# Kernel optimization log

Hardware: AMD Instinct MI355X
Metric: run time of the kernel (lower is better)

The kernel has to match this reference:

```python
import jax, jax.numpy as jnp
import numpy as np

B, T_V, T_A = 128, 64, 128
E_V, E_A = 1024, 512
H, EMB, C = 1024, 512, 512  # C = input_size - embedding_size
IN = EMB + C               # RNN input size = 1024
VOCAB = 20000


def setup_inputs() -> dict:
    key = jax.random.key(0)
    ks = jax.random.split(key, 26)
    s = 0.02
    inp = {
        "input": jax.random.normal(ks[0], (B, 1, EMB), jnp.float32),
        "enc_visual": jax.random.normal(ks[1], (B, T_V, E_V), jnp.float32),
        "enc_audio": jax.random.normal(ks[2], (B, T_A, E_A), jnp.float32),
        "hidden_state": jax.random.normal(ks[3], (1, B, H), jnp.float32),
        "cell_state": jax.random.normal(ks[4], (1, B, H), jnp.float32),
        # visual attention (Bahdanau): W1:[C,H], W2:[C,E_V], W3:[1,C]
        "W_va1": s * jax.random.normal(ks[5], (C, H), jnp.float32),
        "W_va2": s * jax.random.normal(ks[6], (C, E_V), jnp.float32),
        "W_va3": s * jax.random.normal(ks[7], (1, C), jnp.float32),
        "W_venc": s * jax.random.normal(ks[8], (C, E_V), jnp.float32),
        # audio attention
        "W_aa1": s * jax.random.normal(ks[9], (C, H), jnp.float32),
        "W_aa2": s * jax.random.normal(ks[10], (C, E_A), jnp.float32),
        "W_aa3": s * jax.random.normal(ks[11], (1, C), jnp.float32),
        "W_aenc": s * jax.random.normal(ks[12], (C, E_A), jnp.float32),
        # cross-modal context attention (over 2 context vectors)
        "W_ca1": s * jax.random.normal(ks[13], (C, H), jnp.float32),
        "W_ca2": s * jax.random.normal(ks[14], (C, C), jnp.float32),
        "W_ca3": s * jax.random.normal(ks[15], (1, C), jnp.float32),
        # LSTM-style custom RNN cell params
        "W_ih": s * jax.random.normal(ks[16], (4 * H, IN), jnp.float32),
        "W_hh": s * jax.random.normal(ks[17], (4 * H, H), jnp.float32),
        "b_ih": jnp.zeros((4 * H,), jnp.float32),
        "b_hh": jnp.zeros((4 * H,), jnp.float32),
        # output projection
        "W_out": s * jax.random.normal(ks[18], (VOCAB, H), jnp.float32),
        "b_out": jnp.zeros((VOCAB,), jnp.float32),
    }
    return inp


def _attend(h, enc, W1, W2, W3):
    # h: [B,H]; enc: [B,T,E]. Vectorized Bahdanau attention (original loops over T).
    v1 = h @ W1.T                               # [B,C]
    v2 = jnp.einsum('bte,ce->btc', enc, W2)     # [B,T,C]
    scores = jnp.tanh(v1[:, None, :] + v2) @ W3.T  # [B,T,1]
    attn = jax.nn.softmax(scores[..., 0], axis=1)  # [B,T]
    return jnp.einsum('bt,bte->be', attn, enc)     # [B,E]


def reference(input, enc_visual, enc_audio, hidden_state, cell_state,
              W_va1, W_va2, W_va3, W_venc,
              W_aa1, W_aa2, W_aa3, W_aenc,
              W_ca1, W_ca2, W_ca3,
              W_ih, W_hh, b_ih, b_hh, W_out, b_out):
    h0 = hidden_state[0]   # [B,H]
    c0 = cell_state[0]     # [B,H]

    vc = _attend(h0, enc_visual, W_va1, W_va2, W_va3) @ W_venc.T  # [B,C]
    ac = _attend(h0, enc_audio, W_aa1, W_aa2, W_aa3) @ W_aenc.T   # [B,C]
    all_ctx = jnp.stack([vc, ac], axis=1)                         # [B,2,C]
    final_ctx = _attend(h0, all_ctx, W_ca1, W_ca2, W_ca3)         # [B,C]

    x = jnp.concatenate([input[:, 0, :], jnp.tanh(final_ctx)], axis=-1)  # [B,IN]
    gates = x @ W_ih.T + b_ih + h0 @ W_hh.T + b_hh                 # [B,4H]
    i, f, g, o = jnp.split(gates, 4, axis=-1)
    c_new = jax.nn.sigmoid(f) * c0 + jax.nn.sigmoid(i) * jnp.tanh(g)
    h_new = jax.nn.sigmoid(o) * jnp.tanh(c_new)

    logits = h_new @ W_out.T + b_out                               # [B,V]
    return (logits[:, None, :], h_new[None], c_new[None])
```

## Files before the change

kernel.cpp:

```cpp
#include <hip/hip_runtime.h>
#include <hip/hip_bf16.h>
#include <cstddef>

typedef __attribute__((ext_vector_type(8))) short short8;
typedef __attribute__((ext_vector_type(4))) float f32x4;

#define LSTR 40

static __device__ __forceinline__ short8 pack8(float4 f0, float4 f1) {
    union { __hip_bfloat162 h[4]; short8 s; } u;
    u.h[0] = __float22bfloat162_rn(make_float2(f0.x, f0.y));
    u.h[1] = __float22bfloat162_rn(make_float2(f0.z, f0.w));
    u.h[2] = __float22bfloat162_rn(make_float2(f1.x, f1.y));
    u.h[3] = __float22bfloat162_rn(make_float2(f1.z, f1.w));
    return u.s;
}

static __device__ __forceinline__ void sk_body(
    const float* __restrict__ A, int lda,
    const float* __restrict__ W,
    const float* __restrict__ bias, int addbias,
    float* __restrict__ C, int ldc, int N,
    int kbeg, int kend, int n0, int m0)
{
    __shared__ short As[128 * LSTR];
    __shared__ short Ws[64 * LSTR];
    const int tid  = threadIdx.x;
    const int lane = tid & 63;
    const int wave = tid >> 6;
    const int wm = wave * 32;

    f32x4 acc[2][4];
    #pragma unroll
    for (int i = 0; i < 2; ++i)
        #pragma unroll
        for (int j = 0; j < 4; ++j)
            acc[i][j] = (f32x4){0.f, 0.f, 0.f, 0.f};

    const int srow  = tid >> 2;
    const int skoff = (tid & 3) * 8;
    const int frow  = lane & 15;
    const int fkoff = (lane >> 4) * 8;

    for (int k0 = kbeg; k0 < kend; k0 += 32) {
        #pragma unroll
        for (int p = 0; p < 2; ++p) {
            int row = srow + p * 64;
            const float* sa = A + (size_t)(m0 + row) * lda + k0 + skoff;
            *(short8*)(As + row * LSTR + skoff) =
                pack8(*(const float4*)sa, *(const float4*)(sa + 4));
        }
        {
            int n = n0 + srow;
            short8 v = (short8){0,0,0,0,0,0,0,0};
            if (n < N) {
                const float* sw = W + (size_t)n * lda + k0 + skoff;
                v = pack8(*(const float4*)sw, *(const float4*)(sw + 4));
            }
            *(short8*)(Ws + srow * LSTR + skoff) = v;
        }
        __syncthreads();

        short8 af[2], bf[4];
        #pragma unroll
        for (int i = 0; i < 2; ++i)
            af[i] = *(const short8*)(As + (wm + i * 16 + frow) * LSTR + fkoff);
        #pragma unroll
        for (int j = 0; j < 4; ++j)
            bf[j] = *(const short8*)(Ws + (j * 16 + frow) * LSTR + fkoff);
        #pragma unroll
        for (int i = 0; i < 2; ++i)
            #pragma unroll
            for (int j = 0; j < 4; ++j)
                acc[i][j] = __builtin_amdgcn_mfma_f32_16x16x32_bf16(af[i], bf[j], acc[i][j], 0, 0, 0);
        __syncthreads();
    }

    const int cl = lane & 15;
    const int rq = (lane >> 4) * 4;
    #pragma unroll
    for (int j = 0; j < 4; ++j) {
        int gc = n0 + j * 16 + cl;
        if (gc >= N) continue;
        float b = addbias ? bias[gc] : 0.f;
        #pragma unroll
        for (int i = 0; i < 2; ++i) {
            int gr = m0 + wm + i * 16 + rq;
            #pragma unroll
            for (int r = 0; r < 4; ++r)
                atomicAdd(C + (size_t)(gr + r) * ldc + gc, acc[i][j][r] + b);
        }
    }
}

__global__ __launch_bounds__(256) void gemm_sk(
    const float* __restrict__ A, const float* __restrict__ W,
    const float* __restrict__ bias, float* __restrict__ C,
    int N, int K, int kchunk, int ldc)
{
    int kbeg = blockIdx.y * kchunk;
    sk_body(A, K, W, bias, bias != nullptr && blockIdx.y == 0,
            C, ldc, N, kbeg, kbeg + kchunk, blockIdx.x * 64, blockIdx.z * 128);
}

__global__ __launch_bounds__(256) void hproj3_mfma(
    const float* __restrict__ h0,
    const float* __restrict__ Wa, const float* __restrict__ Wb, const float* __restrict__ Wc,
    float* __restrict__ hbase)
{
    int n0g = blockIdx.x * 64;
    int wsel = n0g >> 9;
    const float* W = (wsel == 0) ? Wa : (wsel == 1) ? Wb : Wc;
    float* C = hbase + (size_t)wsel * 128 * 512;
    int kbeg = blockIdx.y * 256;
    sk_body(h0, 1024, W, nullptr, 0, C, 512, 512, kbeg, kbeg + 256, n0g & 511, 0);
}

__global__ __launch_bounds__(256) void ctxproj_mfma(
    const float* __restrict__ attv, const float* __restrict__ Wv,
    const float* __restrict__ atta, const float* __restrict__ Wa,
    float* __restrict__ ctx)
{
    const float* A; const float* W; float* C; int lda, kb, ke;
    if (blockIdx.z == 0) { A = attv; W = Wv; C = ctx;       lda = 1024; kb = blockIdx.y * 256; ke = kb + 256; }
    else                 { A = atta; W = Wa; C = ctx + 512; lda = 512;  kb = blockIdx.y * 128; ke = kb + 128; }
    sk_body(A, lda, W, nullptr, 0, C, 1024, 512, kb, ke, blockIdx.x * 64, 0);
}

__global__ __launch_bounds__(256) void gates_mfma(
    const float* __restrict__ xb, const float* __restrict__ W_ih,
    const float* __restrict__ h0, const float* __restrict__ W_hh,
    float* __restrict__ gates)
{
    int pair = blockIdx.y >> 1;
    const float* A = pair ? h0 : xb;
    const float* W = pair ? W_hh : W_ih;
    int kb = (blockIdx.y & 1) * 512;
    sk_body(A, 1024, W, nullptr, 0, gates, 4096, 4096, kb, kb + 512, blockIdx.x * 64, 0);
}

__global__ __launch_bounds__(256) void gemm_scores(
    const float* __restrict__ A, const float* __restrict__ W,
    const float* __restrict__ v1, const float* __restrict__ W3,
    float* __restrict__ sc, int N, int K, int tshift)
{
    __shared__ short As[128 * LSTR];
    __shared__ short Ws[128 * LSTR];
    const int tid  = threadIdx.x;
    const int lane = tid & 63;
    const int wave = tid >> 6;
    const int m0 = blockIdx.y * 128;
    const int n0 = blockIdx.x * 128;
    const int wm = (wave >> 1) * 64;
    const int wn = (wave & 1) * 64;

    f32x4 acc[4][4];
    #pragma unroll
    for (int i = 0; i < 4; ++i)
        #pragma unroll
        for (int j = 0; j < 4; ++j)
            acc[i][j] = (f32x4){0.f, 0.f, 0.f, 0.f};

    const int srow  = tid >> 2;
    const int skoff = (tid & 3) * 8;
    const int frow  = lane & 15;
    const int fkoff = (lane >> 4) * 8;

    for (int k0 = 0; k0 < K; k0 += 32) {
        #pragma unroll
        for (int p = 0; p < 2; ++p) {
            int row = srow + p * 64;
            const float* sa = A + (size_t)(m0 + row) * K + k0 + skoff;
            *(short8*)(As + row * LSTR + skoff) =
                pack8(*(const float4*)sa, *(const float4*)(sa + 4));
            const float* sw = W + (size_t)(n0 + row) * K + k0 + skoff;
            *(short8*)(Ws + row * LSTR + skoff) =
                pack8(*(const float4*)sw, *(const float4*)(sw + 4));
        }
        __syncthreads();

        short8 af[4], bf[4];
        #pragma unroll
        for (int i = 0; i < 4; ++i)
            af[i] = *(const short8*)(As + (wm + i * 16 + frow) * LSTR + fkoff);
        #pragma unroll
        for (int j = 0; j < 4; ++j)
            bf[j] = *(const short8*)(Ws + (wn + j * 16 + frow) * LSTR + fkoff);
        #pragma unroll
        for (int i = 0; i < 4; ++i)
            #pragma unroll
            for (int j = 0; j < 4; ++j)
                acc[i][j] = __builtin_amdgcn_mfma_f32_16x16x32_bf16(af[i], bf[j], acc[i][j], 0, 0, 0);
        __syncthreads();
    }

    const int cl = lane & 15;
    const int rq = (lane >> 4) * 4;
    #pragma unroll
    for (int i = 0; i < 4; ++i) {
        #pragma unroll
        for (int r = 0; r < 4; ++r) {
            int gr = m0 + wm + i * 16 + rq + r;
            const float* v1row = v1 + (size_t)(gr >> tshift) * 512;
            float p = 0.f;
            #pragma unroll
            for (int j = 0; j < 4; ++j) {
                int gc = n0 + wn + j * 16 + cl;
                p += tanhf(v1row[gc] + acc[i][j][r]) * W3[gc];
            }
            p += __shfl_xor(p, 1, 64);
            p += __shfl_xor(p, 2, 64);
            p += __shfl_xor(p, 4, 64);
            p += __shfl_xor(p, 8, 64);
            if (cl == 0) atomicAdd(sc + gr, p);
        }
    }
}

__global__ __launch_bounds__(256) void attend_out_kernel(
    const float* __restrict__ sc, const float* __restrict__ enc,
    float* __restrict__ out, int T, int E)
{
    __shared__ float raw[128];
    __shared__ float ew[128];
    const int b = blockIdx.x, tid = threadIdx.x;
    if (tid < T) raw[tid] = sc[(size_t)b * T + tid];
    __syncthreads();
    float m = -1e30f;
    for (int t = 0; t < T; ++t) m = fmaxf(m, raw[t]);
    if (tid < T) ew[tid] = __expf(raw[tid] - m);
    __syncthreads();
    float sum = 0.f;
    for (int t = 0; t < T; ++t) sum += ew[t];
    const float inv = 1.f / sum;

    const int e = blockIdx.y * 256 + tid;
    const float* encb = enc + (size_t)b * T * E + e;
    float acc = 0.f;
    for (int t = 0; t < T; ++t)
        acc += ew[t] * encb[(size_t)t * E];
    out[(size_t)b * E + e] = acc * inv;
}

__global__ __launch_bounds__(256) void cross_kernel(
    const float* __restrict__ hc1, const float* __restrict__ v2c,
    const float* __restrict__ W3, const float* __restrict__ ctx,
    const float* __restrict__ inp, float* __restrict__ x)
{
    const int C = 512;
    __shared__ float red[256];
    __shared__ float aw[2];
    const int b = blockIdx.x, tid = threadIdx.x;

    float p0 = 0.f, p1 = 0.f;
    for (int c = tid; c < C; c += 256) {
        float h = hc1[(size_t)b * C + c], w = W3[c];
        p0 += tanhf(h + v2c[(size_t)(b * 2 + 0) * C + c]) * w;
        p1 += tanhf(h + v2c[(size_t)(b * 2 + 1) * C + c]) * w;
    }
    red[tid] = p0; __syncthreads();
    for (int s = 128; s; s >>= 1) { if (tid < s) red[tid] += red[tid + s]; __syncthreads(); }
    float s0 = red[0];
    __syncthreads();
    red[tid] = p1; __syncthreads();
    for (int s = 128; s; s >>= 1) { if (tid < s) red[tid] += red[tid + s]; __syncthreads(); }
    if (tid == 0) {
        float s1 = red[0];
        float m = fmaxf(s0, s1);
        float e0 = __expf(s0 - m), e1 = __expf(s1 - m);
        float inv = 1.f / (e0 + e1);
        aw[0] = e0 * inv; aw[1] = e1 * inv;
    }
    __syncthreads();
    float a0 = aw[0], a1 = aw[1];
    for (int c = tid; c < C; c += 256) {
        float fc = a0 * ctx[(size_t)(b * 2 + 0) * C + c]
                 + a1 * ctx[(size_t)(b * 2 + 1) * C + c];
        x[(size_t)b * 1024 + 512 + c] = tanhf(fc);
        x[(size_t)b * 1024 + c] = inp[(size_t)b * 512 + c];
    }
}

__global__ __launch_bounds__(256) void lstm_kernel(
    const float* __restrict__ gates, const float* __restrict__ c0,
    const float* __restrict__ b_ih, const float* __restrict__ b_hh,
    float* __restrict__ hout, float* __restrict__ cout)
{
    const int idx = blockIdx.x * 256 + threadIdx.x;
    const int b = idx >> 10, h = idx & 1023;
    const float* g = gates + (size_t)b * 4096;
    float gi = g[h]        + b_ih[h]        + b_hh[h];
    float gf = g[1024 + h] + b_ih[1024 + h] + b_hh[1024 + h];
    float gg = g[2048 + h] + b_ih[2048 + h] + b_hh[2048 + h];
    float go = g[3072 + h] + b_ih[3072 + h] + b_hh[3072 + h];
    float si = 1.f / (1.f + __expf(-gi));
    float sf = 1.f / (1.f + __expf(-gf));
    float so = 1.f / (1.f + __expf(-go));
    float cn = sf * c0[idx] + si * tanhf(gg);
    float hn = so * tanhf(cn);
    cout[idx] = cn;
    hout[idx] = hn;
}

extern "C" void kernel_launch(void* const* d_in, const int* in_sizes, int n_in,
                              void* d_out, int out_size, void* d_ws, size_t ws_size,
                              hipStream_t stream)
{
    const float* inp    = (const float*)d_in[0];
    const float* encv   = (const float*)d_in[1];
    const float* enca   = (const float*)d_in[2];
    const float* h0     = (const float*)d_in[3];
    const float* c0     = (const float*)d_in[4];
    const float* W_va1  = (const float*)d_in[5];
    const float* W_va2  = (const float*)d_in[6];
    const float* W_va3  = (const float*)d_in[7];
    const float* W_venc = (const float*)d_in[8];
    const float* W_aa1  = (const float*)d_in[9];
    const float* W_aa2  = (const float*)d_in[10];
    const float* W_aa3  = (const float*)d_in[11];
    const float* W_aenc = (const float*)d_in[12];
    const float* W_ca1  = (const float*)d_in[13];
    const float* W_ca2  = (const float*)d_in[14];
    const float* W_ca3  = (const float*)d_in[15];
    const float* W_ih   = (const float*)d_in[16];
    const float* W_hh   = (const float*)d_in[17];
    const float* b_ih   = (const float*)d_in[18];
    const float* b_hh   = (const float*)d_in[19];
    const float* W_out  = (const float*)d_in[20];
    const float* b_out  = (const float*)d_in[21];
    float* out = (float*)d_out;

    float* ws = (float*)d_ws;
    float* hv1  = ws;  ws += 128 * 512;
    float* ha1  = ws;  ws += 128 * 512;
    float* hc1  = ws;  ws += 128 * 512;
    float* scv  = ws;  ws += 128 * 64;
    float* sca  = ws;  ws += 128 * 128;
    float* ctx  = ws;  ws += 128 * 2 * 512;
    float* v2c  = ws;  ws += 128 * 2 * 512;
    float* gates= ws;  ws += (size_t)128 * 4096;
    size_t zero_floats = (size_t)(ws - (float*)d_ws);
    float* xb   = ws;  ws += 128 * 1024;
    float* attv = ws;  ws += 128 * 1024;
    float* atta = ws;  ws += 128 * 512;

    dim3 blk(256);

    hipMemsetAsync(d_ws, 0, zero_floats * sizeof(float), stream);
    hipMemsetAsync(out, 0, (size_t)128 * 20000 * sizeof(float), stream);

    hproj3_mfma<<<dim3(24, 4), blk, 0, stream>>>(h0, W_va1, W_aa1, W_ca1, hv1);
    gemm_scores<<<dim3(4, 64),  blk, 0, stream>>>(encv, W_va2, hv1, W_va3, scv, 512, 1024, 6);
    gemm_scores<<<dim3(4, 128), blk, 0, stream>>>(enca, W_aa2, ha1, W_aa3, sca, 512,  512, 7);
    attend_out_kernel<<<dim3(128, 4), blk, 0, stream>>>(scv, encv, attv, 64, 1024);
    attend_out_kernel<<<dim3(128, 2), blk, 0, stream>>>(sca, enca, atta, 128, 512);
    ctxproj_mfma<<<dim3(8, 4, 2), blk, 0, stream>>>(attv, W_venc, atta, W_aenc, ctx);
    gemm_sk<<<dim3(8, 2, 2), blk, 0, stream>>>(ctx, W_ca2, nullptr, v2c, 512, 512, 256, 512);
    cross_kernel<<<128, blk, 0, stream>>>(hc1, v2c, W_ca3, ctx, inp, xb);
    gates_mfma<<<dim3(64, 4), blk, 0, stream>>>(xb, W_ih, h0, W_hh, gates);
    float* hout = out + 2560000;
    float* cout = out + 2560000 + 131072;
    lstm_kernel<<<512, blk, 0, stream>>>(gates, c0, b_ih, b_hh, hout, cout);
    gemm_sk<<<dim3(313, 2, 1), blk, 0, stream>>>(hout, W_out, b_out, out, 20000, 1024, 512, 20000);
}
```

Baseline: 457.8 us.

## Merge visual/audio score GEMMs and attend kernels, deepen split-K for small GEMMs

Fuses the two attention score GEMMs into one launch with 64-row M tiles, giving 1536 blocks instead of 768, and fuses the two softmax-weighted sum kernels into one launch. It also doubles the split-K factor for the hidden projection, the context projection, the cross-attention projection and the gates GEMM so more workgroups cover the GPU. This cuts launch count and raises occupancy on the many-CU MI355X. The cost is more atomic accumulation traffic and less reuse of the W tile per block.

```diff
diff --git a/kernel.cpp b/kernel.cpp
--- a/kernel.cpp
+++ b/kernel.cpp
@@ -112,8 +112,8 @@
     int wsel = n0g >> 9;
     const float* W = (wsel == 0) ? Wa : (wsel == 1) ? Wb : Wc;
     float* C = hbase + (size_t)wsel * 128 * 512;
-    int kbeg = blockIdx.y * 256;
-    sk_body(h0, 1024, W, nullptr, 0, C, 512, 512, kbeg, kbeg + 256, n0g & 511, 0);
+    int kbeg = blockIdx.y * 128;
+    sk_body(h0, 1024, W, nullptr, 0, C, 512, 512, kbeg, kbeg + 128, n0g & 511, 0);
 }
 
 __global__ __launch_bounds__(256) void ctxproj_mfma(
@@ -122,8 +122,8 @@
     float* __restrict__ ctx)
 {
     const float* A; const float* W; float* C; int lda, kb, ke;
-    if (blockIdx.z == 0) { A = attv; W = Wv; C = ctx;       lda = 1024; kb = blockIdx.y * 256; ke = kb + 256; }
-    else                 { A = atta; W = Wa; C = ctx + 512; lda = 512;  kb = blockIdx.y * 128; ke = kb + 128; }
+    if (blockIdx.z == 0) { A = attv; W = Wv; C = ctx;       lda = 1024; kb = blockIdx.y * 128; ke = kb + 128; }
+    else                 { A = atta; W = Wa; C = ctx + 512; lda = 512;  kb = blockIdx.y * 64;  ke = kb + 64;  }
     sk_body(A, lda, W, nullptr, 0, C, 1024, 512, kb, ke, blockIdx.x * 64, 0);
 }
 
@@ -132,31 +132,48 @@
     const float* __restrict__ h0, const float* __restrict__ W_hh,
     float* __restrict__ gates)
 {
-    int pair = blockIdx.y >> 1;
+    int pair = blockIdx.y >> 2;
     const float* A = pair ? h0 : xb;
     const float* W = pair ? W_hh : W_ih;
-    int kb = (blockIdx.y & 1) * 512;
-    sk_body(A, 1024, W, nullptr, 0, gates, 4096, 4096, kb, kb + 512, blockIdx.x * 64, 0);
-}
-
-__global__ __launch_bounds__(256) void gemm_scores(
-    const float* __restrict__ A, const float* __restrict__ W,
-    const float* __restrict__ v1, const float* __restrict__ W3,
-    float* __restrict__ sc, int N, int K, int tshift)
-{
-    __shared__ short As[128 * LSTR];
+    int kb = (blockIdx.y & 3) * 256;
+    sk_body(A, 1024, W, nullptr, 0, gates, 4096, 4096, kb, kb + 256, blockIdx.x * 64, 0);
+}
+
+__global__ __launch_bounds__(256) void scores_fused(
+    const float* __restrict__ encv, const float* __restrict__ W_va2,
+    const float* __restrict__ hv1,  const float* __restrict__ W_va3,
+    float* __restrict__ scv,
+    const float* __restrict__ enca, const float* __restrict__ W_aa2,
+    const float* __restrict__ ha1,  const float* __restrict__ W_aa3,
+    float* __restrict__ sca)
+{
+    __shared__ short As[64 * LSTR];
     __shared__ short Ws[128 * LSTR];
+
+    const float *A, *W, *v1, *W3;
+    float* sc;
+    int K, tshift, n0, m0;
+    int idx = blockIdx.x;
+    if (idx < 512) {
+        n0 = (idx >> 7) * 128;  m0 = (idx & 127) * 64;
+        A = encv; W = W_va2; v1 = hv1; W3 = W_va3; sc = scv;
+        K = 1024; tshift = 6;
+    } else {
+        idx -= 512;
+        n0 = (idx >> 8) * 128;  m0 = (idx & 255) * 64;
+        A = enca; W = W_aa2; v1 = ha1; W3 = W_aa3; sc = sca;
+        K = 512; tshift = 7;
+    }
+
     const int tid  = threadIdx.x;
     const int lane = tid & 63;
     const int wave = tid >> 6;
-    const int m0 = blockIdx.y * 128;
-    const int n0 = blockIdx.x * 128;
-    const int wm = (wave >> 1) * 64;
+    const int wm = (wave >> 1) * 32;
     const int wn = (wave & 1) * 64;
 
-    f32x4 acc[4][4];
+    f32x4 acc[2][4];
     #pragma unroll
-    for (int i = 0; i < 4; ++i)
+    for (int i = 0; i < 2; ++i)
         #pragma unroll
         for (int j = 0; j < 4; ++j)
             acc[i][j] = (f32x4){0.f, 0.f, 0.f, 0.f};
@@ -167,27 +184,29 @@
     const int fkoff = (lane >> 4) * 8;
 
     for (int k0 = 0; k0 < K; k0 += 32) {
+        {
+            const float* sa = A + (size_t)(m0 + srow) * K + k0 + skoff;
+            *(short8*)(As + srow * LSTR + skoff) =
+                pack8(*(const float4*)sa, *(const float4*)(sa + 4));
+        }
         #pragma unroll
         for (int p = 0; p < 2; ++p) {
             int row = srow + p * 64;
-            const float* sa = A + (size_t)(m0 + row) * K + k0 + skoff;
-            *(short8*)(As + row * LSTR + skoff) =
-                pack8(*(const float4*)sa, *(const float4*)(sa + 4));
             const float* sw = W + (size_t)(n0 + row) * K + k0 + skoff;
             *(short8*)(Ws + row * LSTR + skoff) =
                 pack8(*(const float4*)sw, *(const float4*)(sw + 4));
         }
         __syncthreads();
 
-        short8 af[4], bf[4];
-        #pragma unroll
-        for (int i = 0; i < 4; ++i)
+        short8 af[2], bf[4];
+        #pragma unroll
+        for (int i = 0; i < 2; ++i)
             af[i] = *(const short8*)(As + (wm + i * 16 + frow) * LSTR + fkoff);
         #pragma unroll
         for (int j = 0; j < 4; ++j)
             bf[j] = *(const short8*)(Ws + (wn + j * 16 + frow) * LSTR + fkoff);
         #pragma unroll
-        for (int i = 0; i < 4; ++i)
+        for (int i = 0; i < 2; ++i)
             #pragma unroll
             for (int j = 0; j < 4; ++j)
                 acc[i][j] = __builtin_amdgcn_mfma_f32_16x16x32_bf16(af[i], bf[j], acc[i][j], 0, 0, 0);
@@ -197,7 +216,7 @@
     const int cl = lane & 15;
     const int rq = (lane >> 4) * 4;
     #pragma unroll
-    for (int i = 0; i < 4; ++i) {
+    for (int i = 0; i < 2; ++i) {
         #pragma unroll
         for (int r = 0; r < 4; ++r) {
             int gr = m0 + wm + i * 16 + rq + r;
@@ -217,13 +236,18 @@
     }
 }
 
-__global__ __launch_bounds__(256) void attend_out_kernel(
-    const float* __restrict__ sc, const float* __restrict__ enc,
-    float* __restrict__ out, int T, int E)
-{
-    __shared__ float raw[128];
+__global__ __launch_bounds__(256) void attend_out2(
+    const float* __restrict__ scv, const float* __restrict__ encv, float* __restrict__ attv,
+    const float* __restrict__ sca, const float* __restrict__ enca, float* __restrict__ atta)
+{
+    const float* sc; const float* enc; float* out;
+    int T, E, ec;
+    if (blockIdx.y < 4) { sc = scv; enc = encv; out = attv; T = 64;  E = 1024; ec = blockIdx.y; }
+    else                { sc = sca; enc = enca; out = atta; T = 128; E = 512;  ec = blockIdx.y - 4; }
+
     __shared__ float ew[128];
     const int b = blockIdx.x, tid = threadIdx.x;
+    __shared__ float raw[128];
     if (tid < T) raw[tid] = sc[(size_t)b * T + tid];
     __syncthreads();
     float m = -1e30f;
@@ -234,7 +258,7 @@
     for (int t = 0; t < T; ++t) sum += ew[t];
     const float inv = 1.f / sum;
 
-    const int e = blockIdx.y * 256 + tid;
+    const int e = ec * 256 + tid;
     const float* encb = enc + (size_t)b * T * E + e;
     float acc = 0.f;
     for (int t = 0; t < T; ++t)
@@ -349,15 +373,14 @@
     hipMemsetAsync(d_ws, 0, zero_floats * sizeof(float), stream);
     hipMemsetAsync(out, 0, (size_t)128 * 20000 * sizeof(float), stream);
 
-    hproj3_mfma<<<dim3(24, 4), blk, 0, stream>>>(h0, W_va1, W_aa1, W_ca1, hv1);
-    gemm_scores<<<dim3(4, 64),  blk, 0, stream>>>(encv, W_va2, hv1, W_va3, scv, 512, 1024, 6);
-    gemm_scores<<<dim3(4, 128), blk, 0, stream>>>(enca, W_aa2, ha1, W_aa3, sca, 512,  512, 7);
-    attend_out_kernel<<<dim3(128, 4), blk, 0, stream>>>(scv, encv, attv, 64, 1024);
-    attend_out_kernel<<<dim3(128, 2), blk, 0, stream>>>(sca, enca, atta, 128, 512);
-    ctxproj_mfma<<<dim3(8, 4, 2), blk, 0, stream>>>(attv, W_venc, atta, W_aenc, ctx);
-    gemm_sk<<<dim3(8, 2, 2), blk, 0, stream>>>(ctx, W_ca2, nullptr, v2c, 512, 512, 256, 512);
+    hproj3_mfma<<<dim3(24, 8), blk, 0, stream>>>(h0, W_va1, W_aa1, W_ca1, hv1);
+    scores_fused<<<dim3(1536), blk, 0, stream>>>(encv, W_va2, hv1, W_va3, scv,
+                                                 enca, W_aa2, ha1, W_aa3, sca);
+    attend_out2<<<dim3(128, 6), blk, 0, stream>>>(scv, encv, attv, sca, enca, atta);
+    ctxproj_mfma<<<dim3(8, 8, 2), blk, 0, stream>>>(attv, W_venc, atta, W_aenc, ctx);
+    gemm_sk<<<dim3(8, 4, 2), blk, 0, stream>>>(ctx, W_ca2, nullptr, v2c, 512, 512, 128, 512);
     cross_kernel<<<128, blk, 0, stream>>>(hc1, v2c, W_ca3, ctx, inp, xb);
-    gates_mfma<<<dim3(64, 4), blk, 0, stream>>>(xb, W_ih, h0, W_hh, gates);
+    gates_mfma<<<dim3(64, 8), blk, 0, stream>>>(xb, W_ih, h0, W_hh, gates);
     float* hout = out + 2560000;
     float* cout = out + 2560000 + 131072;
     lstm_kernel<<<512, blk, 0, stream>>>(gates, c0, b_ih, b_hh, hout, cout);
```

Measured after the change: 397.9 us. -13.1%, faster.
